# Performance work log

Measured on AMD Instinct MI355X. Metric: run time of the kernel, lower is better.

Reference implementation:

```python
import jax, jax.numpy as jnp
import numpy as np

B, C, H, W = 8192, 2048, 2, 2
CR = C // 16
EPS = 1e-5

def setup_inputs() -> dict:
    key = jax.random.key(0)
    ks = jax.random.split(key, 8)
    x = jax.random.normal(ks[0], (B, C, H, W), dtype=jnp.float32)
    gamma = jax.random.normal(ks[1], (C,), dtype=jnp.float32) * 0.1 + 1.0
    beta = jax.random.normal(ks[2], (C,), dtype=jnp.float32) * 0.1
    mean = jax.random.normal(ks[3], (C,), dtype=jnp.float32) * 0.1
    var = jax.random.uniform(ks[4], (C,), dtype=jnp.float32, minval=0.5, maxval=1.5)
    w1 = jax.random.normal(ks[5], (CR, C), dtype=jnp.float32) * (1.0 / np.sqrt(C))
    b1 = jnp.zeros((CR,), dtype=jnp.float32)
    w2 = jax.random.normal(ks[6], (C, CR), dtype=jnp.float32) * (1.0 / np.sqrt(CR))
    b2 = jnp.zeros((C,), dtype=jnp.float32)
    return {"x": x, "gamma": gamma, "beta": beta, "mean": mean, "var": var,
            "w1": w1, "b1": b1, "w2": w2, "b2": b2}

def reference(x, gamma, beta, mean, var, w1, b1, w2, b2):
    # BatchNorm (inference form) + ReLU, over [B,C,H,W]
    inv = gamma * jax.lax.rsqrt(var + EPS)           # [C]
    xn = jax.nn.relu(x * inv[None, :, None, None]
                     + (beta - mean * inv)[None, :, None, None])
    # global average pool -> [B, C]
    p = jnp.mean(xn, axis=(2, 3))
    # two 1x1 convs on [B,C,1,1] == channel MLP
    h = jax.nn.relu(jnp.einsum('bc,rc->br', p, w1) + b1)   # [B, C/16]
    g = jax.nn.sigmoid(jnp.einsum('br,cr->bc', h, w2) + b2) # [B, C]
    # repeat(1,1,2,2) then in-place add == broadcast add over 2x2 spatial
    return x + g[:, :, None, None]
```

## Files before the change

### kernel.cpp

```cpp
#include <hip/hip_runtime.h>


typedef unsigned short u16;
typedef unsigned int u32;
typedef short short8 __attribute__((ext_vector_type(8)));
typedef __bf16 bf16x8 __attribute__((ext_vector_type(8)));
typedef unsigned short ushort4v __attribute__((ext_vector_type(4)));
typedef float floatx4 __attribute__((ext_vector_type(4)));
typedef float floatx2 __attribute__((ext_vector_type(2)));

#define C_CH 2048
#define NB 8
#define THREADS 512
#define PROW 2056
#define HROW 136

#define WS_W2_OFF   (128 * 2048)
#define WS_B1_BYTE  (1u << 20)
#define WS_NEED     ((size_t)(1u << 20) + 512 + 2048 * 4)

__device__ __forceinline__ float bf2f(u16 u) {
    u32 v = ((u32)u) << 16;
    return __builtin_bit_cast(float, v);
}
__device__ __forceinline__ u16 f2bf(float f) {
    u32 v = __builtin_bit_cast(u32, f);
    v = (v + 0x7FFFu + ((v >> 16) & 1u)) >> 16;
    return (u16)v;
}
__device__ __forceinline__ bf16x8 ld8(const u16* p) {
    short8 s = *(const short8*)p;
    return __builtin_bit_cast(bf16x8, s);
}
__device__ __forceinline__ bf16x8 cvt8(floatx4 a, floatx4 b) {
    short8 s;
    s[0] = (short)f2bf(a[0]); s[1] = (short)f2bf(a[1]);
    s[2] = (short)f2bf(a[2]); s[3] = (short)f2bf(a[3]);
    s[4] = (short)f2bf(b[0]); s[5] = (short)f2bf(b[1]);
    s[6] = (short)f2bf(b[2]); s[7] = (short)f2bf(b[3]);
    return __builtin_bit_cast(bf16x8, s);
}
__device__ __forceinline__ bool is_bf16_data(const u16* var_raw) {
    int ok = 1;
    #pragma unroll
    for (int i = 0; i < 8; ++i) {
        u16 u = var_raw[2 * i];
        ok &= (u >= 0x3F00u) && (u <= 0x3FC0u);
    }
    return ok != 0;
}

extern "C" __global__ void __launch_bounds__(256)
se_convw(const void* __restrict__ w1_raw, const void* __restrict__ b1_raw,
         const void* __restrict__ w2_raw, const void* __restrict__ b2_raw,
         const void* __restrict__ var_raw, void* __restrict__ ws) {
    const bool bf = is_bf16_data((const u16*)var_raw);
    u16* w1b = (u16*)ws;
    u16* w2b = w1b + WS_W2_OFF;
    float* b1f = (float*)((char*)ws + WS_B1_BYTE);
    float* b2f = b1f + 128;
    int gid = blockIdx.x * 256 + threadIdx.x;
    if (bf) {
        const ushort4v* s1 = (const ushort4v*)w1_raw;
        const ushort4v* s2 = (const ushort4v*)w2_raw;
        *(ushort4v*)(w1b + gid * 4) = s1[gid];
        *(ushort4v*)(w2b + gid * 4) = s2[gid];
        if (gid < 128)  b1f[gid] = bf2f(((const u16*)b1_raw)[gid]);
        if (gid < 2048) b2f[gid] = bf2f(((const u16*)b2_raw)[gid]);
    } else {
        const floatx4* s1 = (const floatx4*)w1_raw;
        const floatx4* s2 = (const floatx4*)w2_raw;
        floatx4 a = s1[gid], b = s2[gid];
        ushort4v o1, o2;
        #pragma unroll
        for (int j = 0; j < 4; ++j) { o1[j] = f2bf(a[j]); o2[j] = f2bf(b[j]); }
        *(ushort4v*)(w1b + gid * 4) = o1;
        *(ushort4v*)(w2b + gid * 4) = o2;
        if (gid < 128)  b1f[gid] = ((const float*)b1_raw)[gid];
        if (gid < 2048) b2f[gid] = ((const float*)b2_raw)[gid];
    }
}

extern "C" __global__ void __launch_bounds__(THREADS, 8)
se_main(const void* __restrict__ x_raw,
        const void* __restrict__ gamma_raw,
        const void* __restrict__ beta_raw,
        const void* __restrict__ mean_raw,
        const void* __restrict__ var_raw,
        const void* __restrict__ ws,
        void* __restrict__ out_raw) {
    __shared__ u16 p_lds[NB * PROW];
    __shared__ u16 h_lds[NB * HROW];

    const int tid  = threadIdx.x;
    const int lane = tid & 63;
    const int wv   = tid >> 6;
    const int quad = lane >> 4;
    const int l16  = lane & 15;
    const long b0  = (long)blockIdx.x * NB;

    const u16*   w1b = (const u16*)ws;
    const u16*   w2b = w1b + WS_W2_OFF;
    const float* b1f = (const float*)((const char*)ws + WS_B1_BYTE);
    const float* b2f = b1f + 128;

    const bool bf = is_bf16_data((const u16*)var_raw);

    {
        float inv[4], bs[4];
        if (bf) {
            const u16 *gu = (const u16*)gamma_raw, *bu = (const u16*)beta_raw,
                      *mu = (const u16*)mean_raw,  *vu = (const u16*)var_raw;
            #pragma unroll
            for (int k = 0; k < 4; ++k) {
                int c = tid + 512 * k;
                float g = bf2f(gu[c]), bb = bf2f(bu[c]);
                float mm = bf2f(mu[c]), vv = bf2f(vu[c]);
                inv[k] = g * rsqrtf(vv + 1e-5f);
                bs[k]  = bb - mm * inv[k];
            }
        } else {
            const float *gf = (const float*)gamma_raw, *bfp = (const float*)beta_raw,
                        *mf = (const float*)mean_raw,  *vf = (const float*)var_raw;
            #pragma unroll
            for (int k = 0; k < 4; ++k) {
                int c = tid + 512 * k;
                inv[k] = gf[c] * rsqrtf(vf[c] + 1e-5f);
                bs[k]  = bfp[c] - mf[c] * inv[k];
            }
        }
        if (bf) {
            const ushort4v* xr = (const ushort4v*)x_raw + b0 * 2048;
            #pragma unroll 2
            for (int m = 0; m < NB; ++m) {
                #pragma unroll
                for (int k = 0; k < 4; ++k) {
                    int c = tid + 512 * k;
                    ushort4v u = xr[m * 2048 + c];
                    float s = 0.f;
                    #pragma unroll
                    for (int j = 0; j < 4; ++j)
                        s += fmaxf(fmaf(bf2f(u[j]), inv[k], bs[k]), 0.f);
                    p_lds[m * PROW + c] = f2bf(s * 0.25f);
                }
            }
        } else {
            const floatx4* xr = (const floatx4*)x_raw + b0 * 2048;
            #pragma unroll 2
            for (int m = 0; m < NB; ++m) {
                #pragma unroll
                for (int k = 0; k < 4; ++k) {
                    int c = tid + 512 * k;
                    floatx4 v = xr[m * 2048 + c];
                    float s = 0.f;
                    #pragma unroll
                    for (int j = 0; j < 4; ++j)
                        s += fmaxf(fmaf(v[j], inv[k], bs[k]), 0.f);
                    p_lds[m * PROW + c] = f2bf(s * 0.25f);
                }
            }
        }
    }
    __syncthreads();

    const int rr = (wv << 4) | l16;
    {
        floatx4 acc = {0.f, 0.f, 0.f, 0.f};
        const u16* pp  = p_lds + (l16 & 7) * PROW + (quad << 3);
        const u16* w1p = w1b + (long)rr * C_CH + (quad << 3);
        #pragma unroll 4
        for (int k0 = 0; k0 < C_CH; k0 += 32)
            acc = __builtin_amdgcn_mfma_f32_16x16x32_bf16(ld8(pp + k0), ld8(w1p + k0), acc, 0, 0, 0);
        float bb = b1f[rr];
        if (quad < 2) {
            #pragma unroll
            for (int r = 0; r < 4; ++r) {
                int m = (quad << 2) | r;
                h_lds[m * HROW + rr] = f2bf(fmaxf(acc[r] + bb, 0.f));
            }
        }
    }
    __syncthreads();

    {
        bf16x8 af[4];
        #pragma unroll
        for (int kk = 0; kk < 4; ++kk)
            af[kk] = ld8(h_lds + (l16 & 7) * HROW + (kk << 5) + (quad << 3));

        #pragma unroll 2
        for (int i = 0; i < 16; ++i) {
            int c = (wv * 16 + i) * 16 + l16;
            floatx4 a2 = {0.f, 0.f, 0.f, 0.f};
            const u16* w2p = w2b + (long)c * 128 + (quad << 3);
            #pragma unroll
            for (int kk = 0; kk < 4; ++kk)
                a2 = __builtin_amdgcn_mfma_f32_16x16x32_bf16(af[kk], ld8(w2p + (kk << 5)), a2, 0, 0, 0);
            float zb = b2f[c];
            if (quad < 2) {
                #pragma unroll
                for (int r = 0; r < 4; ++r) {
                    int m = (quad << 2) | r;
                    float z = a2[r] + zb;
                    float g = 1.f / (1.f + __expf(-z));
                    p_lds[m * PROW + c] = f2bf(g);
                }
            }
        }
    }
    __syncthreads();

    if (bf) {
        const short8* xr8 = (const short8*)x_raw + b0 * 1024;
        short8*       or8 = (short8*)out_raw + b0 * 1024;
        #pragma unroll 4
        for (int it = 0; it < 16; ++it) {
            int j  = (it << 9) | tid;
            int m  = j >> 10, cc = j & 1023;
            u32 gg = *(const u32*)(&p_lds[m * PROW + (cc << 1)]);
            float g0 = bf2f((u16)gg), g1 = bf2f((u16)(gg >> 16));
            short8 xv = __builtin_nontemporal_load(&xr8[j]);
            short8 ov;
            #pragma unroll
            for (int jj = 0; jj < 4; ++jj) ov[jj] = (short)f2bf(bf2f((u16)xv[jj]) + g0);
            #pragma unroll
            for (int jj = 4; jj < 8; ++jj) ov[jj] = (short)f2bf(bf2f((u16)xv[jj]) + g1);
            __builtin_nontemporal_store(ov, &or8[j]);
        }
    } else {
        const floatx4* xr = (const floatx4*)x_raw + b0 * 2048;
        floatx4*       orr = (floatx4*)out_raw + b0 * 2048;
        #pragma unroll 4
        for (int it = 0; it < 32; ++it) {
            int j = (it << 9) | tid;
            int m = j >> 11, c = j & 2047;
            float g = bf2f(p_lds[m * PROW + c]);
            floatx4 xv = __builtin_nontemporal_load(&xr[j]);
            floatx4 ov = {xv[0] + g, xv[1] + g, xv[2] + g, xv[3] + g};
            __builtin_nontemporal_store(ov, &orr[j]);
        }
    }
}

extern "C" __global__ void __launch_bounds__(THREADS, 8)
se_legacy(const void* __restrict__ x_raw,
          const void* __restrict__ gamma_raw,
          const void* __restrict__ beta_raw,
          const void* __restrict__ mean_raw,
          const void* __restrict__ var_raw,
          const void* __restrict__ w1_raw,
          const void* __restrict__ b1_raw,
          const void* __restrict__ w2_raw,
          const void* __restrict__ b2_raw,
          void* __restrict__ out_raw) {
    __shared__ u16 p_lds[NB * PROW];
    __shared__ u16 h_lds[NB * HROW];

    const int tid  = threadIdx.x;
    const int lane = tid & 63;
    const int wv   = tid >> 6;
    const int quad = lane >> 4;
    const int l16  = lane & 15;
    const long b0  = (long)blockIdx.x * NB;

    const bool bf = is_bf16_data((const u16*)var_raw);

    {
        const int cA = tid << 1;
        const int cB = cA + 1024;
        float gmA0, gmA1, btA0, btA1, mnA0, mnA1, vrA0, vrA1;
        float gmB0, gmB1, btB0, btB1, mnB0, mnB1, vrB0, vrB1;
        if (bf) {
            const u16 *gu = (const u16*)gamma_raw, *bu = (const u16*)beta_raw,
                      *mu = (const u16*)mean_raw,  *vu = (const u16*)var_raw;
            u32 t;
            t = *(const u32*)(gu + cA); gmA0 = bf2f((u16)t); gmA1 = bf2f((u16)(t >> 16));
            t = *(const u32*)(bu + cA); btA0 = bf2f((u16)t); btA1 = bf2f((u16)(t >> 16));
            t = *(const u32*)(mu + cA); mnA0 = bf2f((u16)t); mnA1 = bf2f((u16)(t >> 16));
            t = *(const u32*)(vu + cA); vrA0 = bf2f((u16)t); vrA1 = bf2f((u16)(t >> 16));
            t = *(const u32*)(gu + cB); gmB0 = bf2f((u16)t); gmB1 = bf2f((u16)(t >> 16));
            t = *(const u32*)(bu + cB); btB0 = bf2f((u16)t); btB1 = bf2f((u16)(t >> 16));
            t = *(const u32*)(mu + cB); mnB0 = bf2f((u16)t); mnB1 = bf2f((u16)(t >> 16));
            t = *(const u32*)(vu + cB); vrB0 = bf2f((u16)t); vrB1 = bf2f((u16)(t >> 16));
        } else {
            const float *gf = (const float*)gamma_raw, *bfp = (const float*)beta_raw,
                        *mf = (const float*)mean_raw,  *vf = (const float*)var_raw;
            floatx2 t2;
            t2 = *(const floatx2*)(gf  + cA); gmA0 = t2[0]; gmA1 = t2[1];
            t2 = *(const floatx2*)(bfp + cA); btA0 = t2[0]; btA1 = t2[1];
            t2 = *(const floatx2*)(mf  + cA); mnA0 = t2[0]; mnA1 = t2[1];
            t2 = *(const floatx2*)(vf  + cA); vrA0 = t2[0]; vrA1 = t2[1];
            t2 = *(const floatx2*)(gf  + cB); gmB0 = t2[0]; gmB1 = t2[1];
            t2 = *(const floatx2*)(bfp + cB); btB0 = t2[0]; btB1 = t2[1];
            t2 = *(const floatx2*)(mf  + cB); mnB0 = t2[0]; mnB1 = t2[1];
            t2 = *(const floatx2*)(vf  + cB); vrB0 = t2[0]; vrB1 = t2[1];
        }
        const float invA0 = gmA0 * rsqrtf(vrA0 + 1e-5f), bsA0 = btA0 - mnA0 * invA0;
        const float invA1 = gmA1 * rsqrtf(vrA1 + 1e-5f), bsA1 = btA1 - mnA1 * invA1;
        const float invB0 = gmB0 * rsqrtf(vrB0 + 1e-5f), bsB0 = btB0 - mnB0 * invB0;
        const float invB1 = gmB1 * rsqrtf(vrB1 + 1e-5f), bsB1 = btB1 - mnB1 * invB1;

        if (bf) {
            const short8* x8b = (const short8*)((const u16*)x_raw + b0 * 8192);
            #pragma unroll 2
            for (int m = 0; m < NB; ++m) {
                short8 xa = x8b[(m << 10) + tid];
                short8 xb = x8b[(m << 10) + 512 + tid];
                float sA0 = 0.f, sA1 = 0.f, sB0 = 0.f, sB1 = 0.f;
                #pragma unroll
                for (int j = 0; j < 4; ++j) {
                    sA0 += fmaxf(fmaf(bf2f((u16)xa[j]),     invA0, bsA0), 0.f);
                    sA1 += fmaxf(fmaf(bf2f((u16)xa[4 + j]), invA1, bsA1), 0.f);
                    sB0 += fmaxf(fmaf(bf2f((u16)xb[j]),     invB0, bsB0), 0.f);
                    sB1 += fmaxf(fmaf(bf2f((u16)xb[4 + j]), invB1, bsB1), 0.f);
                }
                *(u32*)(&p_lds[m * PROW + cA]) =
                    (u32)f2bf(sA0 * 0.25f) | ((u32)f2bf(sA1 * 0.25f) << 16);
                *(u32*)(&p_lds[m * PROW + cB]) =
                    (u32)f2bf(sB0 * 0.25f) | ((u32)f2bf(sB1 * 0.25f) << 16);
            }
        } else {
            const floatx4* x4f = (const floatx4*)x_raw + b0 * 2048;
            #pragma unroll 2
            for (int m = 0; m < NB; ++m) {
                int ia = (m << 10) + tid;
                int ib = ia + 512;
                floatx4 a0 = x4f[2 * ia], a1 = x4f[2 * ia + 1];
                floatx4 c0 = x4f[2 * ib], c1 = x4f[2 * ib + 1];
                float sA0 = 0.f, sA1 = 0.f, sB0 = 0.f, sB1 = 0.f;
                #pragma unroll
                for (int j = 0; j < 4; ++j) {
                    sA0 += fmaxf(fmaf(a0[j], invA0, bsA0), 0.f);
                    sA1 += fmaxf(fmaf(a1[j], invA1, bsA1), 0.f);
                    sB0 += fmaxf(fmaf(c0[j], invB0, bsB0), 0.f);
                    sB1 += fmaxf(fmaf(c1[j], invB1, bsB1), 0.f);
                }
                *(u32*)(&p_lds[m * PROW + cA]) =
                    (u32)f2bf(sA0 * 0.25f) | ((u32)f2bf(sA1 * 0.25f) << 16);
                *(u32*)(&p_lds[m * PROW + cB]) =
                    (u32)f2bf(sB0 * 0.25f) | ((u32)f2bf(sB1 * 0.25f) << 16);
            }
        }
    }
    __syncthreads();

    const int rr = (wv << 4) | l16;
    {
        floatx4 acc = {0.f, 0.f, 0.f, 0.f};
        const u16* pp = p_lds + (l16 & 7) * PROW + (quad << 3);
        if (bf) {
            const u16* w1p = (const u16*)w1_raw + (long)rr * C_CH + (quad << 3);
            #pragma unroll 4
            for (int k0 = 0; k0 < C_CH; k0 += 32)
                acc = __builtin_amdgcn_mfma_f32_16x16x32_bf16(ld8(pp + k0), ld8(w1p + k0), acc, 0, 0, 0);
        } else {
            const float* w1p = (const float*)w1_raw + (long)rr * C_CH + (quad << 3);
            #pragma unroll 2
            for (int k0 = 0; k0 < C_CH; k0 += 32) {
                floatx4 wa = *(const floatx4*)(w1p + k0);
                floatx4 wb = *(const floatx4*)(w1p + k0 + 4);
                acc = __builtin_amdgcn_mfma_f32_16x16x32_bf16(ld8(pp + k0), cvt8(wa, wb), acc, 0, 0, 0);
            }
        }
        float bb = bf ? bf2f(((const u16*)b1_raw)[rr]) : ((const float*)b1_raw)[rr];
        if (quad < 2) {
            #pragma unroll
            for (int r = 0; r < 4; ++r) {
                int m = (quad << 2) | r;
                h_lds[m * HROW + rr] = f2bf(fmaxf(acc[r] + bb, 0.f));
            }
        }
    }
    __syncthreads();

    bf16x8 af[4];
    #pragma unroll
    for (int kk = 0; kk < 4; ++kk)
        af[kk] = ld8(h_lds + (l16 & 7) * HROW + (kk << 5) + (quad << 3));

    const ushort4v* x4u = (const ushort4v*)x_raw;
    ushort4v*       o4u = (ushort4v*)out_raw;
    const floatx4*  x4f = (const floatx4*)x_raw;
    floatx4*        o4f = (floatx4*)out_raw;

    for (int i = 0; i < 16; ++i) {
        int c = (wv * 16 + i) * 16 + l16;
        floatx4 a2 = {0.f, 0.f, 0.f, 0.f};
        if (bf) {
            const u16* w2p = (const u16*)w2_raw + (long)c * 128 + (quad << 3);
            #pragma unroll
            for (int kk = 0; kk < 4; ++kk)
                a2 = __builtin_amdgcn_mfma_f32_16x16x32_bf16(af[kk], ld8(w2p + (kk << 5)), a2, 0, 0, 0);
        } else {
            const float* w2p = (const float*)w2_raw + (long)c * 128 + (quad << 3);
            #pragma unroll
            for (int kk = 0; kk < 4; ++kk) {
                floatx4 wa = *(const floatx4*)(w2p + (kk << 5));
                floatx4 wb = *(const floatx4*)(w2p + (kk << 5) + 4);
                a2 = __builtin_amdgcn_mfma_f32_16x16x32_bf16(af[kk], cvt8(wa, wb), a2, 0, 0, 0);
            }
        }
        float zb = bf ? bf2f(((const u16*)b2_raw)[c]) : ((const float*)b2_raw)[c];
        if (quad < 2) {
            #pragma unroll
            for (int r = 0; r < 4; ++r) {
                int m = (quad << 2) | r;
                float z = a2[r] + zb;
                float g = 1.f / (1.f + __expf(-z));
                long idx = (b0 + m) * 2048 + c;
                if (bf) {
                    ushort4v xv = x4u[idx];
                    ushort4v ov;
                    #pragma unroll
                    for (int j = 0; j < 4; ++j) ov[j] = f2bf(bf2f(xv[j]) + g);
                    o4u[idx] = ov;
                } else {
                    floatx4 xv = x4f[idx];
                    floatx4 ov;
                    #pragma unroll
                    for (int j = 0; j < 4; ++j) ov[j] = xv[j] + g;
                    o4f[idx] = ov;
                }
            }
        }
    }
}

extern "C" void kernel_launch(void* const* d_in, const int* in_sizes, int n_in,
                              void* d_out, int out_size, void* d_ws, size_t ws_size,
                              hipStream_t stream) {
    if (d_ws != nullptr && ws_size >= WS_NEED) {
        se_convw<<<dim3(256), dim3(256), 0, stream>>>(
            d_in[5], d_in[6], d_in[7], d_in[8], d_in[4], d_ws);
        se_main<<<dim3(8192 / NB), dim3(THREADS), 0, stream>>>(
            d_in[0], d_in[1], d_in[2], d_in[3], d_in[4], d_ws, d_out);
    } else {
        se_legacy<<<dim3(8192 / NB), dim3(THREADS), 0, stream>>>(
            d_in[0], d_in[1], d_in[2], d_in[3], d_in[4],
            d_in[5], d_in[6], d_in[7], d_in[8], d_out);
    }
}
```

Measured before the change: 544.3 us.

## Split SE into gate kernel with 16-row MFMA tiles and separate residual pass

Adds a gate kernel that handles 16 batch rows per block, so every 16x16 MFMA row is used and weight loads are amortised over twice as many rows. The gate values go to a bf16 workspace buffer, and a second streaming kernel then reads x plus the gate and writes the output. The cost is a second full read of x and an extra round trip of the gate through memory, and the path only runs when the workspace is large enough. The legacy no-workspace kernel is removed, and se_convw now launches even without a workspace.

```diff
diff --git a/kernel.cpp b/kernel.cpp
--- a/kernel.cpp
+++ b/kernel.cpp
@@ -7,17 +7,19 @@
 typedef __bf16 bf16x8 __attribute__((ext_vector_type(8)));
 typedef unsigned short ushort4v __attribute__((ext_vector_type(4)));
 typedef float floatx4 __attribute__((ext_vector_type(4)));
-typedef float floatx2 __attribute__((ext_vector_type(2)));
 
 #define C_CH 2048
-#define NB 8
 #define THREADS 512
+#define NB_G 16
+#define NB_M 8
 #define PROW 2056
 #define HROW 136
 
 #define WS_W2_OFF   (128 * 2048)
 #define WS_B1_BYTE  (1u << 20)
-#define WS_NEED     ((size_t)(1u << 20) + 512 + 2048 * 4)
+#define WS_G_BYTE   (2u << 20)
+#define WS_SMALL_NEED ((size_t)(1u << 20) + 512 + 2048 * 4)
+#define WS_FULL_NEED  ((size_t)(2u << 20) + (size_t)8192 * 2048 * 2)
 
 __device__ __forceinline__ float bf2f(u16 u) {
     u32 v = ((u32)u) << 16;
@@ -30,14 +32,6 @@
 }
 __device__ __forceinline__ bf16x8 ld8(const u16* p) {
     short8 s = *(const short8*)p;
-    return __builtin_bit_cast(bf16x8, s);
-}
-__device__ __forceinline__ bf16x8 cvt8(floatx4 a, floatx4 b) {
-    short8 s;
-    s[0] = (short)f2bf(a[0]); s[1] = (short)f2bf(a[1]);
-    s[2] = (short)f2bf(a[2]); s[3] = (short)f2bf(a[3]);
-    s[4] = (short)f2bf(b[0]); s[5] = (short)f2bf(b[1]);
-    s[6] = (short)f2bf(b[2]); s[7] = (short)f2bf(b[3]);
     return __builtin_bit_cast(bf16x8, s);
 }
 __device__ __forceinline__ bool is_bf16_data(const u16* var_raw) {
@@ -81,28 +75,28 @@
     }
 }
 
-extern "C" __global__ void __launch_bounds__(THREADS, 8)
-se_main(const void* __restrict__ x_raw,
+extern "C" __global__ void __launch_bounds__(THREADS, 4)
+se_gate(const void* __restrict__ x_raw,
         const void* __restrict__ gamma_raw,
         const void* __restrict__ beta_raw,
         const void* __restrict__ mean_raw,
         const void* __restrict__ var_raw,
-        const void* __restrict__ ws,
-        void* __restrict__ out_raw) {
-    __shared__ u16 p_lds[NB * PROW];
-    __shared__ u16 h_lds[NB * HROW];
+        void* __restrict__ ws) {
+    __shared__ u16 p_lds[NB_G * PROW];
+    __shared__ u16 h_lds[NB_G * HROW];
 
     const int tid  = threadIdx.x;
     const int lane = tid & 63;
     const int wv   = tid >> 6;
     const int quad = lane >> 4;
     const int l16  = lane & 15;
-    const long b0  = (long)blockIdx.x * NB;
+    const long b0  = (long)blockIdx.x * NB_G;
 
     const u16*   w1b = (const u16*)ws;
     const u16*   w2b = w1b + WS_W2_OFF;
     const float* b1f = (const float*)((const char*)ws + WS_B1_BYTE);
     const float* b2f = b1f + 128;
+    u16*         g_ws = (u16*)((char*)ws + WS_G_BYTE);
 
     const bool bf = is_bf16_data((const u16*)var_raw);
 
@@ -132,7 +126,7 @@
         if (bf) {
             const ushort4v* xr = (const ushort4v*)x_raw + b0 * 2048;
             #pragma unroll 2
-            for (int m = 0; m < NB; ++m) {
+            for (int m = 0; m < NB_G; ++m) {
                 #pragma unroll
                 for (int k = 0; k < 4; ++k) {
                     int c = tid + 512 * k;
@@ -147,7 +141,173 @@
         } else {
             const floatx4* xr = (const floatx4*)x_raw + b0 * 2048;
             #pragma unroll 2
-            for (int m = 0; m < NB; ++m) {
+            for (int m = 0; m < NB_G; ++m) {
+                #pragma unroll
+                for (int k = 0; k < 4; ++k) {
+                    int c = tid + 512 * k;
+                    floatx4 v = xr[m * 2048 + c];
+                    float s = 0.f;
+                    #pragma unroll
+                    for (int j = 0; j < 4; ++j)
+                        s += fmaxf(fmaf(v[j], inv[k], bs[k]), 0.f);
+                    p_lds[m * PROW + c] = f2bf(s * 0.25f);
+                }
+            }
+        }
+    }
+    __syncthreads();
+
+    const int rr = (wv << 4) | l16;
+    {
+        floatx4 acc = {0.f, 0.f, 0.f, 0.f};
+        const u16* pp  = p_lds + l16 * PROW + (quad << 3);
+        const u16* w1p = w1b + (long)rr * C_CH + (quad << 3);
+        #pragma unroll 4
+        for (int k0 = 0; k0 < C_CH; k0 += 32)
+            acc = __builtin_amdgcn_mfma_f32_16x16x32_bf16(ld8(pp + k0), ld8(w1p + k0), acc, 0, 0, 0);
+        float bb = b1f[rr];
+        #pragma unroll
+        for (int r = 0; r < 4; ++r) {
+            int m = (quad << 2) | r;
+            h_lds[m * HROW + rr] = f2bf(fmaxf(acc[r] + bb, 0.f));
+        }
+    }
+    __syncthreads();
+
+    {
+        bf16x8 af[4];
+        #pragma unroll
+        for (int kk = 0; kk < 4; ++kk)
+            af[kk] = ld8(h_lds + l16 * HROW + (kk << 5) + (quad << 3));
+
+        #pragma unroll 2
+        for (int i = 0; i < 16; ++i) {
+            int c = (wv * 16 + i) * 16 + l16;
+            floatx4 a2 = {0.f, 0.f, 0.f, 0.f};
+            const u16* w2p = w2b + (long)c * 128 + (quad << 3);
+            #pragma unroll
+            for (int kk = 0; kk < 4; ++kk)
+                a2 = __builtin_amdgcn_mfma_f32_16x16x32_bf16(af[kk], ld8(w2p + (kk << 5)), a2, 0, 0, 0);
+            float zb = b2f[c];
+            #pragma unroll
+            for (int r = 0; r < 4; ++r) {
+                int m = (quad << 2) | r;
+                float z = a2[r] + zb;
+                float g = 1.f / (1.f + __expf(-z));
+                g_ws[(b0 + m) * 2048 + c] = f2bf(g);
+            }
+        }
+    }
+}
+
+extern "C" __global__ void __launch_bounds__(THREADS)
+se_resid(const void* __restrict__ x_raw,
+         const void* __restrict__ var_raw,
+         const void* __restrict__ ws,
+         void* __restrict__ out_raw) {
+    const bool bf = is_bf16_data((const u16*)var_raw);
+    const u16* g_ws = (const u16*)((const char*)ws + WS_G_BYTE);
+    const int tid = threadIdx.x;
+
+    if (bf) {
+        const short8* xr  = (const short8*)x_raw;
+        short8*       orr = (short8*)out_raw;
+        const long base = (long)blockIdx.x * 4096;
+        #pragma unroll 4
+        for (int it = 0; it < 8; ++it) {
+            long j = base + it * 512 + tid;
+            u32 gg = *(const u32*)(g_ws + j * 2);
+            float g0 = bf2f((u16)gg), g1 = bf2f((u16)(gg >> 16));
+            short8 xv = xr[j];
+            short8 ov;
+            #pragma unroll
+            for (int jj = 0; jj < 4; ++jj) ov[jj] = (short)f2bf(bf2f((u16)xv[jj]) + g0);
+            #pragma unroll
+            for (int jj = 4; jj < 8; ++jj) ov[jj] = (short)f2bf(bf2f((u16)xv[jj]) + g1);
+            __builtin_nontemporal_store(ov, &orr[j]);
+        }
+    } else {
+        const floatx4* xr  = (const floatx4*)x_raw;
+        floatx4*       orr = (floatx4*)out_raw;
+        const long base = (long)blockIdx.x * 8192;
+        #pragma unroll 4
+        for (int it = 0; it < 16; ++it) {
+            long j = base + it * 512 + tid;
+            float g = bf2f(g_ws[j]);
+            floatx4 xv = xr[j];
+            floatx4 ov = {xv[0] + g, xv[1] + g, xv[2] + g, xv[3] + g};
+            __builtin_nontemporal_store(ov, &orr[j]);
+        }
+    }
+}
+
+extern "C" __global__ void __launch_bounds__(THREADS, 8)
+se_main(const void* __restrict__ x_raw,
+        const void* __restrict__ gamma_raw,
+        const void* __restrict__ beta_raw,
+        const void* __restrict__ mean_raw,
+        const void* __restrict__ var_raw,
+        const void* __restrict__ ws,
+        void* __restrict__ out_raw) {
+    __shared__ u16 p_lds[NB_M * PROW];
+    __shared__ u16 h_lds[NB_M * HROW];
+
+    const int tid  = threadIdx.x;
+    const int lane = tid & 63;
+    const int wv   = tid >> 6;
+    const int quad = lane >> 4;
+    const int l16  = lane & 15;
+    const long b0  = (long)blockIdx.x * NB_M;
+
+    const u16*   w1b = (const u16*)ws;
+    const u16*   w2b = w1b + WS_W2_OFF;
+    const float* b1f = (const float*)((const char*)ws + WS_B1_BYTE);
+    const float* b2f = b1f + 128;
+
+    const bool bf = is_bf16_data((const u16*)var_raw);
+
+    {
+        float inv[4], bs[4];
+        if (bf) {
+            const u16 *gu = (const u16*)gamma_raw, *bu = (const u16*)beta_raw,
+                      *mu = (const u16*)mean_raw,  *vu = (const u16*)var_raw;
+            #pragma unroll
+            for (int k = 0; k < 4; ++k) {
+                int c = tid + 512 * k;
+                float g = bf2f(gu[c]), bb = bf2f(bu[c]);
+                float mm = bf2f(mu[c]), vv = bf2f(vu[c]);
+                inv[k] = g * rsqrtf(vv + 1e-5f);
+                bs[k]  = bb - mm * inv[k];
+            }
+        } else {
+            const float *gf = (const float*)gamma_raw, *bfp = (const float*)beta_raw,
+                        *mf = (const float*)mean_raw,  *vf = (const float*)var_raw;
+            #pragma unroll
+            for (int k = 0; k < 4; ++k) {
+                int c = tid + 512 * k;
+                inv[k] = gf[c] * rsqrtf(vf[c] + 1e-5f);
+                bs[k]  = bfp[c] - mf[c] * inv[k];
+            }
+        }
+        if (bf) {
+            const ushort4v* xr = (const ushort4v*)x_raw + b0 * 2048;
+            #pragma unroll 2
+            for (int m = 0; m < NB_M; ++m) {
+                #pragma unroll
+                for (int k = 0; k < 4; ++k) {
+                    int c = tid + 512 * k;
+                    ushort4v u = xr[m * 2048 + c];
+                    float s = 0.f;
+                    #pragma unroll
+                    for (int j = 0; j < 4; ++j)
+                        s += fmaxf(fmaf(bf2f(u[j]), inv[k], bs[k]), 0.f);
+                    p_lds[m * PROW + c] = f2bf(s * 0.25f);
+                }
+            }
+        } else {
+            const floatx4* xr = (const floatx4*)x_raw + b0 * 2048;
+            #pragma unroll 2
+            for (int m = 0; m < NB_M; ++m) {
                 #pragma unroll
                 for (int k = 0; k < 4; ++k) {
                     int c = tid + 512 * k;
@@ -242,201 +402,18 @@
     }
 }
 
-extern "C" __global__ void __launch_bounds__(THREADS, 8)
-se_legacy(const void* __restrict__ x_raw,
-          const void* __restrict__ gamma_raw,
-          const void* __restrict__ beta_raw,
-          const void* __restrict__ mean_raw,
-          const void* __restrict__ var_raw,
-          const void* __restrict__ w1_raw,
-          const void* __restrict__ b1_raw,
-          const void* __restrict__ w2_raw,
-          const void* __restrict__ b2_raw,
-          void* __restrict__ out_raw) {
-    __shared__ u16 p_lds[NB * PROW];
-    __shared__ u16 h_lds[NB * HROW];
-
-    const int tid  = threadIdx.x;
-    const int lane = tid & 63;
-    const int wv   = tid >> 6;
-    const int quad = lane >> 4;
-    const int l16  = lane & 15;
-    const long b0  = (long)blockIdx.x * NB;
-
-    const bool bf = is_bf16_data((const u16*)var_raw);
-
-    {
-        const int cA = tid << 1;
-        const int cB = cA + 1024;
-        float gmA0, gmA1, btA0, btA1, mnA0, mnA1, vrA0, vrA1;
-        float gmB0, gmB1, btB0, btB1, mnB0, mnB1, vrB0, vrB1;
-        if (bf) {
-            const u16 *gu = (const u16*)gamma_raw, *bu = (const u16*)beta_raw,
-                      *mu = (const u16*)mean_raw,  *vu = (const u16*)var_raw;
-            u32 t;
-            t = *(const u32*)(gu + cA); gmA0 = bf2f((u16)t); gmA1 = bf2f((u16)(t >> 16));
-            t = *(const u32*)(bu + cA); btA0 = bf2f((u16)t); btA1 = bf2f((u16)(t >> 16));
-            t = *(const u32*)(mu + cA); mnA0 = bf2f((u16)t); mnA1 = bf2f((u16)(t >> 16));
-            t = *(const u32*)(vu + cA); vrA0 = bf2f((u16)t); vrA1 = bf2f((u16)(t >> 16));
-            t = *(const u32*)(gu + cB); gmB0 = bf2f((u16)t); gmB1 = bf2f((u16)(t >> 16));
-            t = *(const u32*)(bu + cB); btB0 = bf2f((u16)t); btB1 = bf2f((u16)(t >> 16));
-            t = *(const u32*)(mu + cB); mnB0 = bf2f((u16)t); mnB1 = bf2f((u16)(t >> 16));
-            t = *(const u32*)(vu + cB); vrB0 = bf2f((u16)t); vrB1 = bf2f((u16)(t >> 16));
-        } else {
-            const float *gf = (const float*)gamma_raw, *bfp = (const float*)beta_raw,
-                        *mf = (const float*)mean_raw,  *vf = (const float*)var_raw;
-            floatx2 t2;
-            t2 = *(const floatx2*)(gf  + cA); gmA0 = t2[0]; gmA1 = t2[1];
-            t2 = *(const floatx2*)(bfp + cA); btA0 = t2[0]; btA1 = t2[1];
-            t2 = *(const floatx2*)(mf  + cA); mnA0 = t2[0]; mnA1 = t2[1];
-            t2 = *(const floatx2*)(vf  + cA); vrA0 = t2[0]; vrA1 = t2[1];
-            t2 = *(const floatx2*)(gf  + cB); gmB0 = t2[0]; gmB1 = t2[1];
-            t2 = *(const floatx2*)(bfp + cB); btB0 = t2[0]; btB1 = t2[1];
-            t2 = *(const floatx2*)(mf  + cB); mnB0 = t2[0]; mnB1 = t2[1];
-            t2 = *(const floatx2*)(vf  + cB); vrB0 = t2[0]; vrB1 = t2[1];
-        }
-        const float invA0 = gmA0 * rsqrtf(vrA0 + 1e-5f), bsA0 = btA0 - mnA0 * invA0;
-        const float invA1 = gmA1 * rsqrtf(vrA1 + 1e-5f), bsA1 = btA1 - mnA1 * invA1;
-        const float invB0 = gmB0 * rsqrtf(vrB0 + 1e-5f), bsB0 = btB0 - mnB0 * invB0;
-        const float invB1 = gmB1 * rsqrtf(vrB1 + 1e-5f), bsB1 = btB1 - mnB1 * invB1;
-
-        if (bf) {
-            const short8* x8b = (const short8*)((const u16*)x_raw + b0 * 8192);
-            #pragma unroll 2
-            for (int m = 0; m < NB; ++m) {
-                short8 xa = x8b[(m << 10) + tid];
-                short8 xb = x8b[(m << 10) + 512 + tid];
-                float sA0 = 0.f, sA1 = 0.f, sB0 = 0.f, sB1 = 0.f;
-                #pragma unroll
-                for (int j = 0; j < 4; ++j) {
-                    sA0 += fmaxf(fmaf(bf2f((u16)xa[j]),     invA0, bsA0), 0.f);
-                    sA1 += fmaxf(fmaf(bf2f((u16)xa[4 + j]), invA1, bsA1), 0.f);
-                    sB0 += fmaxf(fmaf(bf2f((u16)xb[j]),     invB0, bsB0), 0.f);
-                    sB1 += fmaxf(fmaf(bf2f((u16)xb[4 + j]), invB1, bsB1), 0.f);
-                }
-                *(u32*)(&p_lds[m * PROW + cA]) =
-                    (u32)f2bf(sA0 * 0.25f) | ((u32)f2bf(sA1 * 0.25f) << 16);
-                *(u32*)(&p_lds[m * PROW + cB]) =
-                    (u32)f2bf(sB0 * 0.25f) | ((u32)f2bf(sB1 * 0.25f) << 16);
-            }
-        } else {
-            const floatx4* x4f = (const floatx4*)x_raw + b0 * 2048;
-            #pragma unroll 2
-            for (int m = 0; m < NB; ++m) {
-                int ia = (m << 10) + tid;
-                int ib = ia + 512;
-                floatx4 a0 = x4f[2 * ia], a1 = x4f[2 * ia + 1];
-                floatx4 c0 = x4f[2 * ib], c1 = x4f[2 * ib + 1];
-                float sA0 = 0.f, sA1 = 0.f, sB0 = 0.f, sB1 = 0.f;
-                #pragma unroll
-                for (int j = 0; j < 4; ++j) {
-                    sA0 += fmaxf(fmaf(a0[j], invA0, bsA0), 0.f);
-                    sA1 += fmaxf(fmaf(a1[j], invA1, bsA1), 0.f);
-                    sB0 += fmaxf(fmaf(c0[j], invB0, bsB0), 0.f);
-                    sB1 += fmaxf(fmaf(c1[j], invB1, bsB1), 0.f);
-                }
-                *(u32*)(&p_lds[m * PROW + cA]) =
-                    (u32)f2bf(sA0 * 0.25f) | ((u32)f2bf(sA1 * 0.25f) << 16);
-                *(u32*)(&p_lds[m * PROW + cB]) =
-                    (u32)f2bf(sB0 * 0.25f) | ((u32)f2bf(sB1 * 0.25f) << 16);
-            }
-        }
-    }
-    __syncthreads();
-
-    const int rr = (wv << 4) | l16;
-    {
-        floatx4 acc = {0.f, 0.f, 0.f, 0.f};
-        const u16* pp = p_lds + (l16 & 7) * PROW + (quad << 3);
-        if (bf) {
-            const u16* w1p = (const u16*)w1_raw + (long)rr * C_CH + (quad << 3);
-            #pragma unroll 4
-            for (int k0 = 0; k0 < C_CH; k0 += 32)
-                acc = __builtin_amdgcn_mfma_f32_16x16x32_bf16(ld8(pp + k0), ld8(w1p + k0), acc, 0, 0, 0);
-        } else {
-            const float* w1p = (const float*)w1_raw + (long)rr * C_CH + (quad << 3);
-            #pragma unroll 2
-            for (int k0 = 0; k0 < C_CH; k0 += 32) {
-                floatx4 wa = *(const floatx4*)(w1p + k0);
-                floatx4 wb = *(const floatx4*)(w1p + k0 + 4);
-                acc = __builtin_amdgcn_mfma_f32_16x16x32_bf16(ld8(pp + k0), cvt8(wa, wb), acc, 0, 0, 0);
-            }
-        }
-        float bb = bf ? bf2f(((const u16*)b1_raw)[rr]) : ((const float*)b1_raw)[rr];
-        if (quad < 2) {
-            #pragma unroll
-            for (int r = 0; r < 4; ++r) {
-                int m = (quad << 2) | r;
-                h_lds[m * HROW + rr] = f2bf(fmaxf(acc[r] + bb, 0.f));
-            }
-        }
-    }
-    __syncthreads();
-
-    bf16x8 af[4];
-    #pragma unroll
-    for (int kk = 0; kk < 4; ++kk)
-        af[kk] = ld8(h_lds + (l16 & 7) * HROW + (kk << 5) + (quad << 3));
-
-    const ushort4v* x4u = (const ushort4v*)x_raw;
-    ushort4v*       o4u = (ushort4v*)out_raw;
-    const floatx4*  x4f = (const floatx4*)x_raw;
-    floatx4*        o4f = (floatx4*)out_raw;
-
-    for (int i = 0; i < 16; ++i) {
-        int c = (wv * 16 + i) * 16 + l16;
-        floatx4 a2 = {0.f, 0.f, 0.f, 0.f};
-        if (bf) {
-            const u16* w2p = (const u16*)w2_raw + (long)c * 128 + (quad << 3);
-            #pragma unroll
-            for (int kk = 0; kk < 4; ++kk)
-                a2 = __builtin_amdgcn_mfma_f32_16x16x32_bf16(af[kk], ld8(w2p + (kk << 5)), a2, 0, 0, 0);
-        } else {
-            const float* w2p = (const float*)w2_raw + (long)c * 128 + (quad << 3);
-            #pragma unroll
-            for (int kk = 0; kk < 4; ++kk) {
-                floatx4 wa = *(const floatx4*)(w2p + (kk << 5));
-                floatx4 wb = *(const floatx4*)(w2p + (kk << 5) + 4);
-                a2 = __builtin_amdgcn_mfma_f32_16x16x32_bf16(af[kk], cvt8(wa, wb), a2, 0, 0, 0);
-            }
-        }
-        float zb = bf ? bf2f(((const u16*)b2_raw)[c]) : ((const float*)b2_raw)[c];
-        if (quad < 2) {
-            #pragma unroll
-            for (int r = 0; r < 4; ++r) {
-                int m = (quad << 2) | r;
-                float z = a2[r] + zb;
-                float g = 1.f / (1.f + __expf(-z));
-                long idx = (b0 + m) * 2048 + c;
-                if (bf) {
-                    ushort4v xv = x4u[idx];
-                    ushort4v ov;
-                    #pragma unroll
-                    for (int j = 0; j < 4; ++j) ov[j] = f2bf(bf2f(xv[j]) + g);
-                    o4u[idx] = ov;
-                } else {
-                    floatx4 xv = x4f[idx];
-                    floatx4 ov;
-                    #pragma unroll
-                    for (int j = 0; j < 4; ++j) ov[j] = xv[j] + g;
-                    o4f[idx] = ov;
-                }
-            }
-        }
-    }
-}
-
 extern "C" void kernel_launch(void* const* d_in, const int* in_sizes, int n_in,
                               void* d_out, int out_size, void* d_ws, size_t ws_size,
                               hipStream_t stream) {
-    if (d_ws != nullptr && ws_size >= WS_NEED) {
-        se_convw<<<dim3(256), dim3(256), 0, stream>>>(
-            d_in[5], d_in[6], d_in[7], d_in[8], d_in[4], d_ws);
-        se_main<<<dim3(8192 / NB), dim3(THREADS), 0, stream>>>(
+    se_convw<<<dim3(256), dim3(256), 0, stream>>>(
+        d_in[5], d_in[6], d_in[7], d_in[8], d_in[4], d_ws);
+    if (d_ws != nullptr && ws_size >= WS_FULL_NEED) {
+        se_gate<<<dim3(8192 / NB_G), dim3(THREADS), 0, stream>>>(
+            d_in[0], d_in[1], d_in[2], d_in[3], d_in[4], d_ws);
+        se_resid<<<dim3(2048), dim3(THREADS), 0, stream>>>(
+            d_in[0], d_in[4], d_ws, d_out);
+    } else {
+        se_main<<<dim3(8192 / NB_M), dim3(THREADS), 0, stream>>>(
             d_in[0], d_in[1], d_in[2], d_in[3], d_in[4], d_ws, d_out);
-    } else {
-        se_legacy<<<dim3(8192 / NB), dim3(THREADS), 0, stream>>>(
-            d_in[0], d_in[1], d_in[2], d_in[3], d_in[4],
-            d_in[5], d_in[6], d_in[7], d_in[8], d_out);
-    }
-}
+    }
+}
```

Result: slower. 559.3 us (+2.8%).
